# Kernel optimization log

Measured on AMD Instinct MI355X. Metric: run time of the kernel, lower is better.

Reference implementation:

```python
import jax, jax.numpy as jnp
import numpy as np

HEAD, D_MODEL, D_KV = 16, 1024, 64
B, NQ, NK = 2, 2048, 2048


def setup_inputs() -> dict:
    key = jax.random.key(0)
    ks = jax.random.split(key, 10)
    s = 1.0 / np.sqrt(D_MODEL)
    return {
        "queries": jax.random.normal(ks[0], (B, NQ, D_MODEL), jnp.float32),
        "keys": jax.random.normal(ks[1], (B, NK, D_MODEL), jnp.float32),
        "values": jax.random.normal(ks[2], (B, NK, D_MODEL), jnp.float32),
        "group_prob": jax.random.uniform(ks[3], (B, 1, NQ, NK), jnp.float32),
        "attention_mask": jnp.ones((B, NK), jnp.int32),
        "Wq": jax.random.normal(ks[4], (D_MODEL, HEAD * D_KV), jnp.float32) * s,
        "bq": jnp.zeros((HEAD * D_KV,), jnp.float32),
        "Wk": jax.random.normal(ks[5], (D_MODEL, HEAD * D_KV), jnp.float32) * s,
        "bk": jnp.zeros((HEAD * D_KV,), jnp.float32),
        "Wv": jax.random.normal(ks[6], (D_MODEL, HEAD * D_KV), jnp.float32) * s,
        "bv": jnp.zeros((HEAD * D_KV,), jnp.float32),
    }


def reference(queries, keys, values, group_prob, attention_mask, Wq, bq, Wk, bk, Wv, bv):
    b_s, nq, _ = queries.shape
    nk = keys.shape[1]
    # projections -> [b, h, n, d]
    q = (queries @ Wq + bq).reshape(b_s, nq, HEAD, D_KV).transpose(0, 2, 1, 3)
    k = (keys @ Wk + bk).reshape(b_s, nk, HEAD, D_KV).transpose(0, 2, 1, 3)
    v = (values @ Wv + bv).reshape(b_s, nk, HEAD, D_KV).transpose(0, 2, 1, 3)
    att = jnp.einsum("bhqd,bhkd->bhqk", q, k) / np.sqrt(D_KV).astype(np.float32)
    # NOTE: original uses non-in-place `att.masked_fill(...)` and discards the
    # result, so attention_mask has NO effect on the computation. Replicated.
    att = jax.nn.softmax(att, axis=-1)
    att = att * group_prob  # post-softmax group gating, broadcast over heads
    out = jnp.einsum("bhqk,bhkd->bhqd", att, v)
    return out.transpose(0, 2, 1, 3).reshape(b_s, nq, D_MODEL)
```

## Files before the change

kernel.cpp:

```cpp
#include <hip/hip_runtime.h>
#include <hip/hip_bf16.h>
#include <cstdint>

typedef unsigned short ushort_t;
typedef __attribute__((ext_vector_type(8))) short short8;
typedef __attribute__((ext_vector_type(4))) short short4v;
typedef __attribute__((ext_vector_type(4))) float floatx4;
typedef __attribute__((ext_vector_type(4))) unsigned int uintx4;
typedef __attribute__((ext_vector_type(4))) unsigned short ushort4_t;

#define H_   16
#define DKV_ 64
#define DM_  1024
#define B_   2
#define NQ_  2048
#define NK_  2048

__device__ __forceinline__ unsigned short f2bf(float f) {
  union { float f; unsigned int u; } v; v.f = f;
  unsigned int u = v.u;
  return (unsigned short)((u + 0x7fffu + ((u >> 16) & 1u)) >> 16);
}

__device__ __forceinline__ float fexp2(float x) { return __builtin_amdgcn_exp2f(x); }
__device__ __forceinline__ float frcp(float x)  { return __builtin_amdgcn_rcpf(x); }

__device__ __forceinline__ unsigned int cvt_pk_bf16(float lo, float hi) {
  unsigned int r;
  asm("v_cvt_pk_bf16_f32 %0, %1, %2" : "=v"(r) : "v"(lo), "v"(hi));
  return r;
}

__device__ __forceinline__ floatx4 mfma16(short8 a, short8 b, floatx4 c) {
  return __builtin_amdgcn_mfma_f32_16x16x32_bf16(a, b, c, 0, 0, 0);
}

__device__ __forceinline__ void gload_lds16(const ushort_t* g, ushort_t* l) {
  __builtin_amdgcn_global_load_lds(
      (const __attribute__((address_space(1))) void*)g,
      (__attribute__((address_space(3))) void*)l, 16, 0, 0);
}

__global__ __launch_bounds__(256) void cast_x_kernel(
    const float* __restrict__ q, const float* __restrict__ k,
    const float* __restrict__ v, ushort_t* __restrict__ dst)
{
  const int t = blockIdx.y;
  const float* src = (t == 0) ? q : (t == 1) ? k : v;
  ushort_t* d = dst + (size_t)t * 4096 * 1024;
  const int gid = blockIdx.x * 256 + threadIdx.x;
  #pragma unroll
  for (int u = 0; u < 8; u++) {
    const int i4 = u * 131072 + gid;
    floatx4 f = ((const floatx4*)src)[i4];
    ushort4_t o;
    #pragma unroll
    for (int e = 0; e < 4; e++) o[e] = f2bf(f[e]);
    *(ushort4_t*)&d[(size_t)i4 * 4] = o;
  }
}

__global__ __launch_bounds__(256) void cast_wt_kernel(
    const float* __restrict__ Wq, const float* __restrict__ Wk,
    const float* __restrict__ Wv, ushort_t* __restrict__ WtAll)
{
  __shared__ ushort_t tile[32][33];
  const int t = blockIdx.z;
  const float* W = (t == 0) ? Wq : (t == 1) ? Wk : Wv;
  ushort_t* Wt = WtAll + (size_t)t * 1024 * 1024;
  const int n0 = blockIdx.x * 32, k0 = blockIdx.y * 32;
  const int tid = threadIdx.x, r = tid >> 3, c4 = (tid & 7) * 4;
  floatx4 f = *(const floatx4*)&W[(size_t)(k0 + r) * 1024 + n0 + c4];
  #pragma unroll
  for (int e = 0; e < 4; e++) tile[r][c4 + e] = f2bf(f[e]);
  __syncthreads();
  ushort4_t o;
  #pragma unroll
  for (int e = 0; e < 4; e++) o[e] = tile[c4 + e][r];
  *(ushort4_t*)&Wt[(size_t)(n0 + r) * 1024 + k0 + c4] = o;
}

__global__ __launch_bounds__(256, 2) void proj_kernel2(
    const ushort_t* __restrict__ Xbf, const ushort_t* __restrict__ WtAll,
    const float* __restrict__ bq, const float* __restrict__ bk,
    const float* __restrict__ bv,
    ushort_t* __restrict__ Qb, ushort_t* __restrict__ Kb, ushort_t* __restrict__ Vt)
{
  const int mode = blockIdx.z;
  const ushort_t* X  = Xbf  + (size_t)mode * 4096 * 1024;
  const ushort_t* Wt = WtAll + (size_t)mode * 1024 * 1024;
  const float* bias  = (mode == 0) ? bq : (mode == 1) ? bk : bv;
  ushort_t* dst      = (mode == 0) ? Qb : (mode == 1) ? Kb : Vt;

  __shared__ ushort_t SM[8192];
  ushort_t* SA = SM;
  ushort_t* SB = SM + 4096;

  const int tid = threadIdx.x, lane = tid & 63, wid = tid >> 6;
  const int c = lane & 15, g = lane >> 4;
  const int m0 = blockIdx.y * 128, n0 = blockIdx.x * 128;
  const int wm = wid & 1, wn = wid >> 1, mb = wm * 64, nb = wn * 64;
  const int srow = lane >> 2;
  const int schunk = (lane & 3) * 8;

  floatx4 acc[4][4];
  #pragma unroll
  for (int i = 0; i < 4; i++)
    #pragma unroll
    for (int j = 0; j < 4; j++) acc[i][j] = floatx4{0.f, 0.f, 0.f, 0.f};

  for (int k0 = 0; k0 < DM_; k0 += 32) {
    __syncthreads();
    #pragma unroll
    for (int u = 0; u < 2; u++) {
      const int t = wid * 2 + u;
      gload_lds16(&X [(size_t)(m0 + t * 16 + srow) * 1024 + k0 + schunk], &SA[t * 512]);
      gload_lds16(&Wt[(size_t)(n0 + t * 16 + srow) * 1024 + k0 + schunk], &SB[t * 512]);
    }
    __syncthreads();

    short8 af[4], bfr[4];
    #pragma unroll
    for (int i = 0; i < 4; i++) af[i]  = *(const short8*)&SA[(mb + i * 16 + c) * 32 + g * 8];
    #pragma unroll
    for (int j = 0; j < 4; j++) bfr[j] = *(const short8*)&SB[(nb + j * 16 + c) * 32 + g * 8];
    #pragma unroll
    for (int i = 0; i < 4; i++)
      #pragma unroll
      for (int j = 0; j < 4; j++) acc[i][j] = mfma16(af[i], bfr[j], acc[i][j]);
  }

  __syncthreads();
  const float scale = (mode == 0) ? 0.18033688011112042f : 1.0f;
  ushort_t* EP = SM + wid * 2048;
  const int hh = (n0 + nb) >> 6;

  if (mode != 2) {
    for (int jj = 0; jj < 2; jj++) {
      #pragma unroll
      for (int jt = 0; jt < 2; jt++) {
        const int j = jj * 2 + jt;
        const float bb = bias[n0 + nb + j * 16 + c];
        #pragma unroll
        for (int i = 0; i < 4; i++)
          #pragma unroll
          for (int r = 0; r < 4; r++)
            EP[(i * 16 + g * 4 + r) * 32 + jt * 16 + c] =
                f2bf((acc[i][j][r] + bb) * scale);
      }
      #pragma unroll
      for (int u = 0; u < 8; u++) {
        const int rowl = u * 8 + (lane >> 3);
        ushort4_t vv = *(ushort4_t*)&EP[rowl * 32 + (lane & 7) * 4];
        const int rowg = m0 + mb + rowl;
        const int bb2 = rowg >> 11, nn = rowg & 2047;
        *(ushort4_t*)&dst[((size_t)(bb2 * H_ + hh) * NQ_ + nn) * DKV_ +
                          jj * 32 + (lane & 7) * 4] = vv;
      }
    }
  } else {
    const int bb2 = (m0 + mb) >> 11, nloc = (m0 + mb) & 2047;
    for (int j = 0; j < 4; j++) {
      const float bb = bias[n0 + nb + j * 16 + c];
      #pragma unroll
      for (int i = 0; i < 4; i++) {
        ushort4_t pk;
        #pragma unroll
        for (int r = 0; r < 4; r++) pk[r] = f2bf(acc[i][j][r] + bb);
        *(ushort4_t*)&EP[c * 72 + i * 16 + g * 4] = pk;
      }
      const int d0 = j * 16;
      #pragma unroll
      for (int u = 0; u < 2; u++) {
        const int coll = u * 8 + (lane >> 3);
        short8 vv = *(const short8*)&EP[coll * 72 + (lane & 7) * 8];
        *(short8*)&dst[((size_t)(bb2 * H_ + hh) * DKV_ + d0 + coll) * NK_ +
                       nloc + (lane & 7) * 8] = vv;
      }
    }
  }
}

constexpr int LDT = 40;
__global__ __launch_bounds__(256, 2) void proj_kernel_fb(
    const float* __restrict__ Xq, const float* __restrict__ Xk, const float* __restrict__ Xv,
    const float* __restrict__ Wq, const float* __restrict__ Wk, const float* __restrict__ Wv,
    const float* __restrict__ bq, const float* __restrict__ bk, const float* __restrict__ bv,
    ushort_t* __restrict__ Qb, ushort_t* __restrict__ Kb, ushort_t* __restrict__ Vt)
{
  const int mode = blockIdx.z;
  const float* X    = (mode == 0) ? Xq : (mode == 1) ? Xk : Xv;
  const float* W    = (mode == 0) ? Wq : (mode == 1) ? Wk : Wv;
  const float* bias = (mode == 0) ? bq : (mode == 1) ? bk : bv;
  ushort_t* dst     = (mode == 0) ? Qb : (mode == 1) ? Kb : Vt;

  __shared__ ushort_t Asm[128 * LDT];
  __shared__ ushort_t Bsm[128 * LDT];

  const int tid = threadIdx.x, lane = tid & 63, wid = tid >> 6;
  const int m0 = blockIdx.y * 128, n0 = blockIdx.x * 128;
  const int c = lane & 15, g = lane >> 4;
  const int wm = wid & 1, wn = wid >> 1, mb = wm * 64, nb = wn * 64;

  floatx4 acc[4][4];
  #pragma unroll
  for (int i = 0; i < 4; i++)
    #pragma unroll
    for (int j = 0; j < 4; j++) acc[i][j] = floatx4{0.f, 0.f, 0.f, 0.f};

  const int ar = tid >> 1, ah = tid & 1;
  const int bn = tid & 127, bh2 = tid >> 7;

  for (int k0 = 0; k0 < DM_; k0 += 32) {
    const floatx4* ap = (const floatx4*)(X + (size_t)(m0 + ar) * DM_ + k0 + ah * 16);
    floatx4 av0 = ap[0], av1 = ap[1], av2 = ap[2], av3 = ap[3];
    const float* wp = W + (size_t)(k0 + bh2 * 16) * 1024 + n0 + bn;
    float wv[16];
    #pragma unroll
    for (int j = 0; j < 16; j++) wv[j] = wp[j * 1024];
    short8 pa0, pa1, pb0, pb1;
    #pragma unroll
    for (int j = 0; j < 4; j++) {
      pa0[j] = (short)f2bf(av0[j]); pa0[4 + j] = (short)f2bf(av1[j]);
      pa1[j] = (short)f2bf(av2[j]); pa1[4 + j] = (short)f2bf(av3[j]);
    }
    #pragma unroll
    for (int j = 0; j < 8; j++) { pb0[j] = (short)f2bf(wv[j]); pb1[j] = (short)f2bf(wv[8 + j]); }
    __syncthreads();
    *(short8*)&Asm[ar * LDT + ah * 16]      = pa0;
    *(short8*)&Asm[ar * LDT + ah * 16 + 8]  = pa1;
    *(short8*)&Bsm[bn * LDT + bh2 * 16]     = pb0;
    *(short8*)&Bsm[bn * LDT + bh2 * 16 + 8] = pb1;
    __syncthreads();
    short8 af[4], bfr[4];
    #pragma unroll
    for (int i = 0; i < 4; i++) af[i]  = *(const short8*)&Asm[(mb + i * 16 + c) * LDT + g * 8];
    #pragma unroll
    for (int j = 0; j < 4; j++) bfr[j] = *(const short8*)&Bsm[(nb + j * 16 + c) * LDT + g * 8];
    #pragma unroll
    for (int i = 0; i < 4; i++)
      #pragma unroll
      for (int j = 0; j < 4; j++) acc[i][j] = mfma16(af[i], bfr[j], acc[i][j]);
  }
  #pragma unroll
  for (int j = 0; j < 4; j++) {
    const int col = n0 + nb + j * 16 + c;
    const float bv_ = bias[col];
    const int h = col >> 6, d = col & 63;
    #pragma unroll
    for (int i = 0; i < 4; i++)
      #pragma unroll
      for (int r = 0; r < 4; r++) {
        const int row = m0 + mb + i * 16 + g * 4 + r;
        const int b = row >> 11, n = row & 2047;
        float v = acc[i][j][r] + bv_;
        if (mode == 0) {
          v *= 0.18033688011112042f;
          dst[((size_t)(b * H_ + h) * NQ_ + n) * DKV_ + d] = f2bf(v);
        } else if (mode == 1) {
          dst[((size_t)(b * H_ + h) * NQ_ + n) * DKV_ + d] = f2bf(v);
        } else {
          dst[((size_t)(b * H_ + h) * DKV_ + d) * NK_ + n] = f2bf(v);
        }
      }
  }
}

__global__ __launch_bounds__(512, 4) void attn_kernel(
    const ushort_t* __restrict__ Qb, const ushort_t* __restrict__ Kb,
    const ushort_t* __restrict__ Vt, const float* __restrict__ gp,
    float* __restrict__ out)
{
  __shared__ ushort_t Ks[2][64 * 72];
  __shared__ ushort_t Vs[2][64 * 72];

  const int tid = threadIdx.x, lane = tid & 63, wid = tid >> 6;
  const int c = lane & 15, g = lane >> 4;
  const int h = blockIdx.x, b = blockIdx.z;
  const int bh = b * H_ + h;
  const int qw = blockIdx.y * 128 + wid * 16;

  const ushort_t* Qp = Qb + (size_t)bh * NQ_ * DKV_;
  const ushort_t* Kp = Kb + (size_t)bh * NK_ * DKV_;
  const ushort_t* Vp = Vt + (size_t)bh * DKV_ * NK_;
  const float* gpq = gp + (size_t)b * NQ_ * NK_ + (size_t)(qw + c) * NK_;

  const int srow = tid >> 3;
  const int u    = tid & 7;
  const int scol = u * 8;
  const int so_lo = 32 * (u >> 2) + 8 * ((2 * u) & 3) + 4 * ((u >> 1) & 1);
  const int so_hi = 32 * (u >> 2) + 8 * ((2 * u + 1) & 3) + 4 * ((u >> 1) & 1);

  short8 qf[2];
  #pragma unroll
  for (int kc = 0; kc < 2; kc++)
    qf[kc] = *(const short8*)&Qp[(qw + c) * DKV_ + kc * 32 + g * 8];

  *(short8*)&Ks[0][srow * 72 + scol] = *(const short8*)&Kp[(size_t)srow * DKV_ + scol];
  {
    short8 v8 = *(const short8*)&Vp[(size_t)srow * NK_ + scol];
    short4v vlo, vhi;
    #pragma unroll
    for (int e = 0; e < 4; e++) { vlo[e] = v8[e]; vhi[e] = v8[4 + e]; }
    *(short4v*)&Vs[0][srow * 72 + so_lo] = vlo;
    *(short4v*)&Vs[0][srow * 72 + so_hi] = vhi;
  }
  __syncthreads();

  floatx4 o[4];
  float l = 0.f;
  #pragma unroll
  for (int jd = 0; jd < 4; jd++) o[jd] = floatx4{0.f, 0.f, 0.f, 0.f};

  for (int t = 0; t < NK_ / 64; t++) {
    const int k0 = t * 64;
    const int cur = t & 1, nxt = cur ^ 1;

    floatx4 gpv[4];
    #pragma unroll
    for (int jk = 0; jk < 4; jk++)
      gpv[jk] = *(const floatx4*)&gpq[k0 + jk * 16 + g * 4];

    short8 knx;
    short4v vlo, vhi;
    const bool has_next = (t + 1) < NK_ / 64;
    if (has_next) {
      const int k1 = k0 + 64;
      knx = *(const short8*)&Kp[(size_t)(k1 + srow) * DKV_ + scol];
      short8 v8 = *(const short8*)&Vp[(size_t)srow * NK_ + k1 + scol];
      #pragma unroll
      for (int e = 0; e < 4; e++) { vlo[e] = v8[e]; vhi[e] = v8[4 + e]; }
    }

    floatx4 s[4];
    #pragma unroll
    for (int jk = 0; jk < 4; jk++) {
      s[jk] = floatx4{0.f, 0.f, 0.f, 0.f};
      #pragma unroll
      for (int kc = 0; kc < 2; kc++) {
        short8 kf = *(const short8*)&Ks[cur][(jk * 16 + c) * 72 + kc * 32 + g * 8];
        s[jk] = mfma16(kf, qf[kc], s[jk]);
      }
    }

    uintx4 afw[2];
    #pragma unroll
    for (int jk = 0; jk < 4; jk++) {
      const float p0 = fexp2(s[jk][0]);
      const float p1 = fexp2(s[jk][1]);
      const float p2 = fexp2(s[jk][2]);
      const float p3 = fexp2(s[jk][3]);
      l += (p0 + p1) + (p2 + p3);
      const unsigned int w0 = cvt_pk_bf16(p0 * gpv[jk][0], p1 * gpv[jk][1]);
      const unsigned int w1 = cvt_pk_bf16(p2 * gpv[jk][2], p3 * gpv[jk][3]);
      afw[jk >> 1][2 * (jk & 1) + 0] = w0;
      afw[jk >> 1][2 * (jk & 1) + 1] = w1;
    }

    #pragma unroll
    for (int kc = 0; kc < 2; kc++) {
      const short8 af = __builtin_bit_cast(short8, afw[kc]);
      #pragma unroll
      for (int jd = 0; jd < 4; jd++) {
        short8 vf = *(const short8*)&Vs[cur][(jd * 16 + c) * 72 + kc * 32 + g * 8];
        o[jd] = mfma16(af, vf, o[jd]);
      }
    }

    if (has_next) {
      *(short8*)&Ks[nxt][srow * 72 + scol] = knx;
      *(short4v*)&Vs[nxt][srow * 72 + so_lo] = vlo;
      *(short4v*)&Vs[nxt][srow * 72 + so_hi] = vhi;
    }
    __syncthreads();
  }

  float lf = l;
  lf += __shfl_xor(lf, 16);
  lf += __shfl_xor(lf, 32);
  const float inv = frcp(lf);
  float invr[4];
  #pragma unroll
  for (int r = 0; r < 4; r++) invr[r] = __shfl(inv, g * 4 + r);

  #pragma unroll
  for (int jd = 0; jd < 4; jd++)
    #pragma unroll
    for (int r = 0; r < 4; r++) {
      const int row = qw + g * 4 + r;
      out[(size_t)(b * NQ_ + row) * 1024 + h * 64 + jd * 16 + c] =
          o[jd][r] * invr[r];
    }
}

extern "C" void kernel_launch(void* const* d_in, const int* in_sizes, int n_in,
                              void* d_out, int out_size, void* d_ws, size_t ws_size,
                              hipStream_t stream) {
  const float* queries = (const float*)d_in[0];
  const float* keys    = (const float*)d_in[1];
  const float* values  = (const float*)d_in[2];
  const float* gp      = (const float*)d_in[3];
  const float* Wq = (const float*)d_in[5];
  const float* bq = (const float*)d_in[6];
  const float* Wk = (const float*)d_in[7];
  const float* bk = (const float*)d_in[8];
  const float* Wv = (const float*)d_in[9];
  const float* bv = (const float*)d_in[10];

  const size_t SZ_QKV = (size_t)3 * B_ * H_ * NQ_ * DKV_;
  const size_t SZ_X   = (size_t)3 * 4096 * 1024;
  const size_t SZ_W   = (size_t)3 * 1024 * 1024;
  const size_t NEED   = (SZ_QKV + SZ_X + SZ_W) * sizeof(ushort_t);

  ushort_t* Qb = (ushort_t*)d_ws;
  ushort_t* Kb = Qb + (size_t)B_ * H_ * NQ_ * DKV_;
  ushort_t* Vt = Kb + (size_t)B_ * H_ * NK_ * DKV_;
  float* out = (float*)d_out;

  if (ws_size >= NEED) {
    ushort_t* Xbf = Qb + SZ_QKV;
    ushort_t* Wt  = Xbf + SZ_X;
    cast_x_kernel<<<dim3(512, 3), 256, 0, stream>>>(queries, keys, values, Xbf);
    cast_wt_kernel<<<dim3(32, 32, 3), 256, 0, stream>>>(Wq, Wk, Wv, Wt);
    proj_kernel2<<<dim3(8, 32, 3), 256, 0, stream>>>(
        Xbf, Wt, bq, bk, bv, Qb, Kb, Vt);
  } else {
    proj_kernel_fb<<<dim3(8, 32, 3), 256, 0, stream>>>(
        queries, keys, values, Wq, Wk, Wv, bq, bk, bv, Qb, Kb, Vt);
  }
  attn_kernel<<<dim3(H_, NQ_ / 128, B_), 512, 0, stream>>>(Qb, Kb, Vt, gp, out);
}
```

Baseline: 255.1 us.

## Split attention key range across two wave groups and merge partials in LDS

Each block now handles 64 queries with two 4-wave groups that each process half of the key sequence in 32-key tiles. The partial outputs and row sums are combined through shared memory at the end. K tiles are loaded directly from global memory into LDS with an XOR swizzle, and the occupancy hint is raised. The goal is more parallel blocks and fewer register and LDS stalls, at the cost of an extra reduction step and a barrier.

```diff
diff --git a/kernel.cpp b/kernel.cpp
--- a/kernel.cpp
+++ b/kernel.cpp
@@ -266,44 +266,54 @@
   }
 }
 
-__global__ __launch_bounds__(512, 4) void attn_kernel(
+__global__ __launch_bounds__(512, 8) void attn_kernel(
     const ushort_t* __restrict__ Qb, const ushort_t* __restrict__ Kb,
     const ushort_t* __restrict__ Vt, const float* __restrict__ gp,
     float* __restrict__ out)
 {
-  __shared__ ushort_t Ks[2][64 * 72];
-  __shared__ ushort_t Vs[2][64 * 72];
-
-  const int tid = threadIdx.x, lane = tid & 63, wid = tid >> 6;
+  __shared__ ushort_t SMEM[2][9216];
+
+  constexpr int NT = 32;
+
+  const int tid = threadIdx.x, lane = tid & 63;
+  const int wid = tid >> 6;
+  const int grp = wid >> 2;
+  const int wid4 = wid & 3;
   const int c = lane & 15, g = lane >> 4;
   const int h = blockIdx.x, b = blockIdx.z;
   const int bh = b * H_ + h;
-  const int qw = blockIdx.y * 128 + wid * 16;
+  const int qw = blockIdx.y * 64 + wid4 * 16;
+  const int kbase = grp << 10;
 
   const ushort_t* Qp = Qb + (size_t)bh * NQ_ * DKV_;
   const ushort_t* Kp = Kb + (size_t)bh * NK_ * DKV_;
   const ushort_t* Vp = Vt + (size_t)bh * DKV_ * NK_;
   const float* gpq = gp + (size_t)b * NQ_ * NK_ + (size_t)(qw + c) * NK_;
 
-  const int srow = tid >> 3;
-  const int u    = tid & 7;
-  const int scol = u * 8;
-  const int so_lo = 32 * (u >> 2) + 8 * ((2 * u) & 3) + 4 * ((u >> 1) & 1);
-  const int so_hi = 32 * (u >> 2) + 8 * ((2 * u + 1) & 3) + 4 * ((u >> 1) & 1);
-
-  short8 qf[2];
-  #pragma unroll
-  for (int kc = 0; kc < 2; kc++)
-    qf[kc] = *(const short8*)&Qp[(qw + c) * DKV_ + kc * 32 + g * 8];
-
-  *(short8*)&Ks[0][srow * 72 + scol] = *(const short8*)&Kp[(size_t)srow * DKV_ + scol];
+  ushort_t* KsG = &SMEM[grp][0];
+  ushort_t* VsG = &SMEM[grp][4096];
+
+  const int tid2 = tid & 255;
+  const int srow = tid2 >> 2;
+  const int u    = tid2 & 3;
+  const int so_lo = 8 * ((2 * u) & 3) + 4 * ((u >> 1) & 1);
+  const int so_hi = 8 * ((2 * u + 1) & 3) + 4 * ((u >> 1) & 1);
+  const int krow = wid4 * 8 + (lane >> 3);
+  const int kscg = (lane & 7) ^ ((lane >> 3) & 7);
+  const int kcol0 = ((0 + g) ^ (c & 7)) << 3;
+  const int kcol1 = ((4 + g) ^ (c & 7)) << 3;
+
+  const short8 qf0 = *(const short8*)&Qp[(qw + c) * DKV_ + g * 8];
+  const short8 qf1 = *(const short8*)&Qp[(qw + c) * DKV_ + 32 + g * 8];
+
+  gload_lds16(&Kp[(size_t)(kbase + krow) * DKV_ + kscg * 8], &KsG[wid4 * 512]);
   {
-    short8 v8 = *(const short8*)&Vp[(size_t)srow * NK_ + scol];
-    short4v vlo, vhi;
-    #pragma unroll
-    for (int e = 0; e < 4; e++) { vlo[e] = v8[e]; vhi[e] = v8[4 + e]; }
-    *(short4v*)&Vs[0][srow * 72 + so_lo] = vlo;
-    *(short4v*)&Vs[0][srow * 72 + so_hi] = vhi;
+    short8 v8 = *(const short8*)&Vp[(size_t)srow * NK_ + kbase + u * 8];
+    short4v vl, vh;
+    #pragma unroll
+    for (int e = 0; e < 4; e++) { vl[e] = v8[e]; vh[e] = v8[4 + e]; }
+    *(short4v*)&VsG[srow * 40 + so_lo] = vl;
+    *(short4v*)&VsG[srow * 40 + so_hi] = vh;
   }
   __syncthreads();
 
@@ -312,85 +322,88 @@
   #pragma unroll
   for (int jd = 0; jd < 4; jd++) o[jd] = floatx4{0.f, 0.f, 0.f, 0.f};
 
-  for (int t = 0; t < NK_ / 64; t++) {
-    const int k0 = t * 64;
+  for (int t = 0; t < NT; ++t) {
     const int cur = t & 1, nxt = cur ^ 1;
-
-    floatx4 gpv[4];
-    #pragma unroll
-    for (int jk = 0; jk < 4; jk++)
-      gpv[jk] = *(const floatx4*)&gpq[k0 + jk * 16 + g * 4];
-
-    short8 knx;
-    short4v vlo, vhi;
-    const bool has_next = (t + 1) < NK_ / 64;
-    if (has_next) {
-      const int k1 = k0 + 64;
-      knx = *(const short8*)&Kp[(size_t)(k1 + srow) * DKV_ + scol];
-      short8 v8 = *(const short8*)&Vp[(size_t)srow * NK_ + k1 + scol];
-      #pragma unroll
-      for (int e = 0; e < 4; e++) { vlo[e] = v8[e]; vhi[e] = v8[4 + e]; }
-    }
-
-    floatx4 s[4];
-    #pragma unroll
-    for (int jk = 0; jk < 4; jk++) {
-      s[jk] = floatx4{0.f, 0.f, 0.f, 0.f};
-      #pragma unroll
-      for (int kc = 0; kc < 2; kc++) {
-        short8 kf = *(const short8*)&Ks[cur][(jk * 16 + c) * 72 + kc * 32 + g * 8];
-        s[jk] = mfma16(kf, qf[kc], s[jk]);
-      }
-    }
-
-    uintx4 afw[2];
-    #pragma unroll
-    for (int jk = 0; jk < 4; jk++) {
-      const float p0 = fexp2(s[jk][0]);
-      const float p1 = fexp2(s[jk][1]);
-      const float p2 = fexp2(s[jk][2]);
-      const float p3 = fexp2(s[jk][3]);
-      l += (p0 + p1) + (p2 + p3);
-      const unsigned int w0 = cvt_pk_bf16(p0 * gpv[jk][0], p1 * gpv[jk][1]);
-      const unsigned int w1 = cvt_pk_bf16(p2 * gpv[jk][2], p3 * gpv[jk][3]);
-      afw[jk >> 1][2 * (jk & 1) + 0] = w0;
-      afw[jk >> 1][2 * (jk & 1) + 1] = w1;
-    }
-
-    #pragma unroll
-    for (int kc = 0; kc < 2; kc++) {
-      const short8 af = __builtin_bit_cast(short8, afw[kc]);
-      #pragma unroll
-      for (int jd = 0; jd < 4; jd++) {
-        short8 vf = *(const short8*)&Vs[cur][(jd * 16 + c) * 72 + kc * 32 + g * 8];
-        o[jd] = mfma16(af, vf, o[jd]);
-      }
-    }
-
-    if (has_next) {
-      *(short8*)&Ks[nxt][srow * 72 + scol] = knx;
-      *(short4v*)&Vs[nxt][srow * 72 + so_lo] = vlo;
-      *(short4v*)&Vs[nxt][srow * 72 + so_hi] = vhi;
+    const int k0 = kbase + t * 32;
+    const bool hn = (t + 1) < NT;
+
+    if (hn)
+      gload_lds16(&Kp[(size_t)(k0 + 32 + krow) * DKV_ + kscg * 8],
+                  &KsG[nxt * 2048 + wid4 * 512]);
+    short8 vr = {};
+    if (hn) vr = *(const short8*)&Vp[(size_t)srow * NK_ + k0 + 32 + u * 8];
+
+    const floatx4 gp0 = *(const floatx4*)&gpq[k0 + g * 4];
+    const floatx4 gp1 = *(const floatx4*)&gpq[k0 + 16 + g * 4];
+
+    const ushort_t* Kc = &KsG[cur * 2048];
+    const ushort_t* Vc = &VsG[cur * 2560];
+    floatx4 s0 = floatx4{0.f, 0.f, 0.f, 0.f};
+    floatx4 s1 = floatx4{0.f, 0.f, 0.f, 0.f};
+    s0 = mfma16(*(const short8*)&Kc[(c) * 64 + kcol0], qf0, s0);
+    s0 = mfma16(*(const short8*)&Kc[(c) * 64 + kcol1], qf1, s0);
+    s1 = mfma16(*(const short8*)&Kc[(16 + c) * 64 + kcol0], qf0, s1);
+    s1 = mfma16(*(const short8*)&Kc[(16 + c) * 64 + kcol1], qf1, s1);
+
+    const float p00 = fexp2(s0[0]), p01 = fexp2(s0[1]);
+    const float p02 = fexp2(s0[2]), p03 = fexp2(s0[3]);
+    const float p10 = fexp2(s1[0]), p11 = fexp2(s1[1]);
+    const float p12 = fexp2(s1[2]), p13 = fexp2(s1[3]);
+    l += ((p00 + p01) + (p02 + p03)) + ((p10 + p11) + (p12 + p13));
+    const unsigned int w0 = cvt_pk_bf16(p00 * gp0[0], p01 * gp0[1]);
+    const unsigned int w1 = cvt_pk_bf16(p02 * gp0[2], p03 * gp0[3]);
+    const unsigned int w2 = cvt_pk_bf16(p10 * gp1[0], p11 * gp1[1]);
+    const unsigned int w3 = cvt_pk_bf16(p12 * gp1[2], p13 * gp1[3]);
+    const uintx4 aw = uintx4{w0, w1, w2, w3};
+    const short8 af = __builtin_bit_cast(short8, aw);
+
+    #pragma unroll
+    for (int jd = 0; jd < 4; jd++) {
+      short8 vf = *(const short8*)&Vc[(jd * 16 + c) * 40 + g * 8];
+      o[jd] = mfma16(af, vf, o[jd]);
+    }
+
+    if (hn) {
+      short4v vl, vh;
+      #pragma unroll
+      for (int e = 0; e < 4; e++) { vl[e] = vr[e]; vh[e] = vr[4 + e]; }
+      *(short4v*)&VsG[nxt * 2560 + srow * 40 + so_lo] = vl;
+      *(short4v*)&VsG[nxt * 2560 + srow * 40 + so_hi] = vh;
     }
     __syncthreads();
   }
 
-  float lf = l;
-  lf += __shfl_xor(lf, 16);
-  lf += __shfl_xor(lf, 32);
-  const float inv = frcp(lf);
-  float invr[4];
-  #pragma unroll
-  for (int r = 0; r < 4; r++) invr[r] = __shfl(inv, g * 4 + r);
-
-  #pragma unroll
-  for (int jd = 0; jd < 4; jd++)
-    #pragma unroll
-    for (int r = 0; r < 4; r++) {
-      const int row = qw + g * 4 + r;
-      out[(size_t)(b * NQ_ + row) * 1024 + h * 64 + jd * 16 + c] =
-          o[jd][r] * invr[r];
-    }
+  float* M = (float*)&SMEM[0][0];
+  if (grp == 1) {
+    const int mi = (wid4 * 64 + lane) * 17;
+    #pragma unroll
+    for (int jd = 0; jd < 4; jd++) *(floatx4*)&M[mi + jd * 4] = o[jd];
+    M[mi + 16] = l;
+  }
+  __syncthreads();
+  if (grp == 0) {
+    const int mi = (wid4 * 64 + lane) * 17;
+    #pragma unroll
+    for (int jd = 0; jd < 4; jd++) o[jd] += *(const floatx4*)&M[mi + jd * 4];
+    l += M[mi + 16];
+
+    float lf = l;
+    lf += __shfl_xor(lf, 16);
+    lf += __shfl_xor(lf, 32);
+    const float inv = frcp(lf);
+    float invr[4];
+    #pragma unroll
+    for (int r = 0; r < 4; r++) invr[r] = __shfl(inv, g * 4 + r);
+
+    #pragma unroll
+    for (int jd = 0; jd < 4; jd++)
+      #pragma unroll
+      for (int r = 0; r < 4; r++) {
+        const int row = qw + g * 4 + r;
+        out[(size_t)(b * NQ_ + row) * 1024 + h * 64 + jd * 16 + c] =
+            o[jd][r] * invr[r];
+      }
+  }
 }
 
 extern "C" void kernel_launch(void* const* d_in, const int* in_sizes, int n_in,
@@ -428,5 +441,5 @@
     proj_kernel_fb<<<dim3(8, 32, 3), 256, 0, stream>>>(
         queries, keys, values, Wq, Wk, Wv, bq, bk, bv, Qb, Kb, Vt);
   }
-  attn_kernel<<<dim3(H_, NQ_ / 128, B_), 512, 0, stream>>>(Qb, Kb, Vt, gp, out);
-}
+  attn_kernel<<<dim3(H_, NQ_ / 64, B_), 512, 0, stream>>>(Qb, Kb, Vt, gp, out);
+}
```

After: 265.9 us. 1.04x slower.
